# Kernel tuning notes

Measured on AMD Instinct MI355X. Metric: run time of the kernel, lower is better.

The kernel has to match this reference:

```python
import jax, jax.numpy as jnp
import numpy as np

B, N, C = 8, 89, 1024
H = C // 2  # adaptor hidden dim = channel_in // 2


def _mlp2(t, W1, b1, W2, b2):
    # MLP(channel_in, [channel_in, channel_out]): Linear -> ReLU -> Linear
    return jax.nn.relu(t @ W1 + b1) @ W2 + b2


def setup_inputs() -> dict:
    key = jax.random.key(0)
    ks = jax.random.split(key, 12)
    g = lambda k, shape, fan: jax.random.normal(k, shape, jnp.float32) * (fan ** -0.5)
    return {
        "x": jax.random.normal(ks[0], (B, N, C), jnp.float32),
        # two independently learned dense adjacencies (AddConv / ModulatorConv)
        "adj_add": jax.random.normal(ks[1], (N, N), jnp.float32),
        "adj_mod": jax.random.normal(ks[2], (N, N), jnp.float32),
        # Adaptor MLP: C -> C -> H -> 1
        "Wa1": g(ks[3], (C, C), C), "ba1": jnp.zeros((C,), jnp.float32),
        "Wa2": g(ks[4], (C, H), C), "ba2": jnp.zeros((H,), jnp.float32),
        "Wa3": g(ks[5], (H, 1), H), "ba3": jnp.zeros((1,), jnp.float32),
        # mlp_add: C -> C -> C
        "Wadd1": g(ks[6], (C, C), C), "badd1": jnp.zeros((C,), jnp.float32),
        "Wadd2": g(ks[7], (C, C), C), "badd2": jnp.zeros((C,), jnp.float32),
        # mlp_mod: C -> C -> C
        "Wmod1": g(ks[8], (C, C), C), "bmod1": jnp.zeros((C,), jnp.float32),
        "Wmod2": g(ks[9], (C, C), C), "bmod2": jnp.zeros((C,), jnp.float32),
    }


def reference(x, adj_add, adj_mod, Wa1, ba1, Wa2, ba2, Wa3, ba3,
              Wadd1, badd1, Wadd2, badd2, Wmod1, bmod1, Wmod2, bmod2):
    # dense_to_sparse on an all-nonzero learned randn adj => fully connected graph;
    # PyG convention: edge_index[0]=row=source j, edge_index[1]=col=target i,
    # so aggregation at node i sums over adj[j, i] * message(j -> i).

    # Adaptor: per-edge gate s_{b,j,i} = sigmoid(MLP(x_j * x_i))
    p = x[:, :, None, :] * x[:, None, :, :]              # [B, Nsrc, Ndst, C]
    h = jax.nn.relu(p @ Wa1 + ba1)                       # [B, N, N, C]
    h = jax.nn.relu(h @ Wa2 + ba2)                       # [B, N, N, H]
    s = jax.nn.sigmoid((h @ Wa3 + ba3)[..., 0])          # [B, Nsrc, Ndst]

    # AddConv: out[b,i,f] = sum_j s[b,j,i] * adj_add[j,i] * x[b,j,f]
    a_t = jnp.einsum('bji,ji,bjf->bif', s, adj_add, x)
    # ModulatorConv: out[b,i,f] = x[b,i,f] * sum_j adj_mod[j,i] * x[b,j,f]
    m_t = x * jnp.einsum('ji,bjf->bif', adj_mod, x)

    out_add = _mlp2(a_t, Wadd1, badd1, Wadd2, badd2)
    out_mod = _mlp2(m_t, Wmod1, bmod1, Wmod2, bmod2)
    return (x + out_add + out_mod) / 3.0
```

## Files before the change

### kernel.cpp

```cpp
#include <hip/hip_runtime.h>

typedef unsigned short u16;
typedef unsigned int   u32;
typedef __attribute__((ext_vector_type(8))) short bf16x8;
typedef __attribute__((ext_vector_type(4))) float f32x4;

#define DEVFN __device__ __forceinline__

DEVFN float b2f(u16 u){ u32 t=((u32)u)<<16; float f; __builtin_memcpy(&f,&t,4); return f; }
DEVFN u16 f2b(float f){ u32 t; __builtin_memcpy(&t,&f,4); t += 0x7fffu + ((t>>16)&1u); return (u16)(t>>16); }
DEVFN u32 pk2(float a, float b){ return (u32)f2b(a) | ((u32)f2b(b)<<16); }

DEVFN void row2ji(int row, int* jj, int* ii){
  int j = (int)((179.0f - sqrtf(179.0f*179.0f - 8.0f*(float)row)) * 0.5f);
  if(j < 0) j = 0; if(j > 88) j = 88;
  while(j < 88 && (j+1)*(179-(j+1))/2 <= row) j++;
  while(j > 0 && j*(179-j)/2 > row) j--;
  *jj = j;
  *ii = j + (row - j*(179-j)/2);
}

struct TrArgs { const float* src; u16* dst; int C; };
struct TrPack { TrArgs a[6]; };

__global__ __launch_bounds__(256) void prep_k(TrPack pk, float* __restrict__ logit,
                                              float* __restrict__ dout,
                                              const float* __restrict__ x,
                                              u16* __restrict__ pbuf, long pz){
  __shared__ u16 tile[32][33];
  int id = blockIdx.x, tid = threadIdx.x;
  if(id < 6144){
    TrArgs t = pk.a[id>>10];
    int q = id & 1023;
    int bx = (q&31)*32, by = (q>>5)*32;
    if(bx >= t.C) return;
    int tx = tid&31, ty = tid>>5;
    #pragma unroll
    for(int yy=ty; yy<32; yy+=8) tile[yy][tx] = f2b(t.src[(size_t)(by+yy)*t.C + bx+tx]);
    __syncthreads();
    #pragma unroll
    for(int yy=ty; yy<32; yy+=8) t.dst[(size_t)(bx+yy)*1024 + by+tx] = tile[tx][yy];
  } else if(id < 6176){
    int idx = (id-6144)*1024 + tid*4;
    *(float4*)(logit + idx) = (float4){0.f,0.f,0.f,0.f};
  } else if(id < 6888){
    int idx = (id-6176)*1024 + tid*4;
    *(float4*)(dout + idx) = (float4){0.f,0.f,0.f,0.f};
  } else {
    int pid = id - 6888;
    int z = pid >> 11, rp = pid & 2047;
    int half = tid >> 7, t7 = tid & 127;
    int row = rp*2 + half;
    int j, i; row2ji(row < 4005 ? row : 0, &j, &i);
    const float* xb = x + (size_t)z*91136;
    int c = t7*8;
    float4 a0 = *(const float4*)(xb + (size_t)j*1024 + c);
    float4 a1 = *(const float4*)(xb + (size_t)j*1024 + c + 4);
    float4 b0 = *(const float4*)(xb + (size_t)i*1024 + c);
    float4 b1 = *(const float4*)(xb + (size_t)i*1024 + c + 4);
    uint4 o;
    o.x = pk2(a0.x*b0.x, a0.y*b0.y);
    o.y = pk2(a0.z*b0.z, a0.w*b0.w);
    o.z = pk2(a1.x*b1.x, a1.y*b1.y);
    o.w = pk2(a1.z*b1.z, a1.w*b1.w);
    *(uint4*)(pbuf + (size_t)z*pz + (size_t)row*1024 + c) = o;
  }
}

__global__ __launch_bounds__(256) void pgen_k(const float* __restrict__ x,
                                              u16* __restrict__ p, long pz, int bbase){
  int z = blockIdx.y, b = bbase + z, row = blockIdx.x;
  int j, i; row2ji(row < 4005 ? row : 0, &j, &i);
  const float* xb = x + (size_t)b*91136;
  int c = threadIdx.x*4;
  float4 a  = *(const float4*)(xb + (size_t)j*1024 + c);
  float4 bb = *(const float4*)(xb + (size_t)i*1024 + c);
  ushort4 o;
  o.x = f2b(a.x*bb.x); o.y = f2b(a.y*bb.y);
  o.z = f2b(a.z*bb.z); o.w = f2b(a.w*bb.w);
  *(ushort4*)(p + (size_t)z*pz + (size_t)row*1024 + c) = o;
}

template<int ROWS>
DEVFN void stage_gl(const u16* __restrict__ g0, u16* lds0, int tid){
  constexpr int IT = ROWS/32;
  int w = tid>>6, lane = tid&63;
  #pragma unroll
  for(int i=0;i<IT;i++){
    int p  = (w*IT+i)*64 + lane;
    int r  = p>>3;
    int kb = (p&7) ^ (r&7);
    const u16* g = g0 + ((size_t)r<<10) + (kb<<3);
    u16* l = lds0 + (size_t)(w*IT+i)*512;
    __builtin_amdgcn_global_load_lds((const __attribute__((address_space(1))) u32*)g,
                                     (__attribute__((address_space(3))) u32*)l, 16, 0, 0);
  }
}

template<int AMODE, int EPI, int TM, int TN, int MINW>
__global__ __launch_bounds__(256,MINW) void gemm_k(
    const u16* __restrict__ A0, const u16* __restrict__ B0,
    const u16* __restrict__ A1, const u16* __restrict__ B1,
    const float* __restrict__ bias0, const float* __restrict__ bias1,
    const float* __restrict__ aux,
    void* __restrict__ out,
    long a0z, long oz, int ldo, int aux2, int kiters,
    int mmask, int mshift, int mlimit)
{
  constexpr int MB = TM/32, NB = TN/32;
  int by = blockIdx.y;
  int m0 = (by & mmask)*TM, n0 = (by >> mshift)*TN, z = blockIdx.z;
  if(m0 >= mlimit) return;

  __shared__ __align__(16) u16 smem[TM*64 + TN*64];
  u16* As = smem;
  u16* Bs = smem + TM*64;
  int tid = threadIdx.x;

  const u16* Abase0;
  const u16* Bbase0;
  if(AMODE==2){
    Abase0 = (z ? A1 : A0) + (size_t)m0*1024;
    Bbase0 = (z ? B1 : B0) + (size_t)n0*1024;
  } else {
    Abase0 = A0 + (size_t)z*a0z + (size_t)m0*1024;
    Bbase0 = B0 + (size_t)n0*1024;
  }

  f32x4 acc[MB][NB];
  #pragma unroll
  for(int a=0;a<MB;a++)
    #pragma unroll
    for(int b=0;b<NB;b++) acc[a][b] = (f32x4){0.f,0.f,0.f,0.f};

  int w = tid>>6, lane = tid&63, quad = lane>>4, l15 = lane&15;
  int wr = (w>>1)*(TM/2), wc = (w&1)*(TN/2);

  for(int kk=0; kk<kiters; kk++){
    int k0 = (kk & 15) << 6;
    const u16* Ab = Abase0 + k0;
    const u16* Bb = Bbase0 + k0;
    __syncthreads();
    stage_gl<TM>(Ab, As, tid);
    stage_gl<TN>(Bb, Bs, tid);
    __syncthreads();
    #pragma unroll
    for(int kq=0; kq<2; kq++){
      int kbl = kq*4 + quad;
      bf16x8 af[MB], bfv[NB];
      #pragma unroll
      for(int t=0;t<MB;t++){
        int rr = wr + t*16 + l15;
        af[t] = *(const bf16x8*)(As + rr*64 + ((kbl ^ (rr&7))<<3));
      }
      #pragma unroll
      for(int t=0;t<NB;t++){
        int cc = wc + t*16 + l15;
        bfv[t] = *(const bf16x8*)(Bs + cc*64 + ((kbl ^ (cc&7))<<3));
      }
      #pragma unroll
      for(int rt=0;rt<MB;rt++)
        #pragma unroll
        for(int ct=0;ct<NB;ct++)
          acc[rt][ct] = __builtin_amdgcn_mfma_f32_16x16x32_bf16(af[rt], bfv[ct], acc[rt][ct], 0,0,0);
    }
  }

  float bc[NB], w3[NB];
  #pragma unroll
  for(int ct=0;ct<NB;ct++){
    int colg = n0 + wc + ct*16 + l15;
    if(EPI==3){
      bc[ct] = (z==0) ? (bias0[colg] + bias1[colg]) : 0.f;
    } else {
      bc[ct] = (AMODE==2 && z) ? bias1[colg] : bias0[colg];
      if(EPI==2) w3[ct] = aux[colg];
    }
  }

  if(EPI==2){
    float part[MB][4];
    #pragma unroll
    for(int rt=0;rt<MB;rt++)
      #pragma unroll
      for(int r=0;r<4;r++) part[rt][r] = 0.f;
    #pragma unroll
    for(int rt=0;rt<MB;rt++)
      #pragma unroll
      for(int ct=0;ct<NB;ct++)
        #pragma unroll
        for(int r=0;r<4;r++)
          part[rt][r] += fmaxf(acc[rt][ct][r] + bc[ct], 0.f) * w3[ct];
    #pragma unroll
    for(int m=1;m<16;m<<=1)
      #pragma unroll
      for(int rt=0;rt<MB;rt++)
        #pragma unroll
        for(int r=0;r<4;r++)
          part[rt][r] += __shfl_xor(part[rt][r], m, 64);
    if(l15==0){
      float* lo = (float*)out + (size_t)(aux2 + z)*4096;
      #pragma unroll
      for(int rt=0;rt<MB;rt++)
        #pragma unroll
        for(int r=0;r<4;r++)
          atomicAdd(lo + (m0 + wr + rt*16 + quad*4 + r), part[rt][r]);
    }
    return;
  }

  if(EPI==3){
    const float third = 1.f/3.f;
    float* op = (float*)out;
    #pragma unroll
    for(int ct=0;ct<NB;ct++){
      int colg = n0 + wc + ct*16 + l15;
      #pragma unroll
      for(int rt=0;rt<MB;rt++){
        #pragma unroll
        for(int r=0;r<4;r++){
          int rowg = m0 + wr + rt*16 + quad*4 + r;
          if(rowg < aux2){
            float v = acc[rt][ct][r];
            if(z==0) v += aux[(size_t)rowg*1024 + colg] + bc[ct];
            atomicAdd(op + (size_t)rowg*ldo + colg, v*third);
          }
        }
      }
    }
    return;
  }

  __syncthreads();
  u16* Ct = smem;
  #pragma unroll
  for(int ct=0;ct<NB;ct++){
    int cl = wc + ct*16 + l15;
    #pragma unroll
    for(int rt=0;rt<MB;rt++){
      #pragma unroll
      for(int r=0;r<4;r++){
        int rl = wr + rt*16 + quad*4 + r;
        Ct[rl*TN + cl] = f2b(fmaxf(acc[rt][ct][r] + bc[ct], 0.f));
      }
    }
  }
  __syncthreads();
  u16* outp = (u16*)out + (size_t)z*oz;
  #pragma unroll
  for(int i=0;i<TM*TN/2048;i++){
    int q = i*256 + tid;
    int row = q/(TN/8), c16 = q%(TN/8);
    *(uint4*)(outp + (size_t)(m0+row)*ldo + n0 + c16*8) = *(const uint4*)(Ct + row*TN + c16*8);
  }
}

__global__ __launch_bounds__(256) void k4_k(const float* __restrict__ x,
    const float* __restrict__ adjA, const float* __restrict__ adjM,
    const float* __restrict__ logit, const float* __restrict__ ba3,
    u16* __restrict__ a_t, u16* __restrict__ m_t)
{
  int b = blockIdx.y, i = blockIdx.x, t = threadIdx.x;
  __shared__ float ca[89], cm[89];
  if(t < 89){
    int tri = (t<=i) ? t*(179-t)/2 + (i-t) : i*(179-i)/2 + (t-i);
    float lg = logit[(size_t)b*4096 + tri] + ba3[0];
    float sv = 1.f/(1.f + expf(-lg));
    ca[t] = sv * adjA[t*89 + i];
    cm[t] = adjM[t*89 + i];
  }
  __syncthreads();
  const float* xb = x + (size_t)b*91136;
  int c0 = t*4;
  float aa0=0,aa1=0,aa2=0,aa3=0, am0=0,am1=0,am2=0,am3=0;
  #pragma unroll 8
  for(int j=0;j<89;j++){
    float4 xv = *(const float4*)(xb + (size_t)j*1024 + c0);
    float fa=ca[j], fm=cm[j];
    aa0+=fa*xv.x; aa1+=fa*xv.y; aa2+=fa*xv.z; aa3+=fa*xv.w;
    am0+=fm*xv.x; am1+=fm*xv.y; am2+=fm*xv.z; am3+=fm*xv.w;
  }
  float4 xi = *(const float4*)(xb + (size_t)i*1024 + c0);
  size_t ro = ((size_t)(b*89 + i))*1024 + c0;
  ushort4 oa; oa.x=f2b(aa0); oa.y=f2b(aa1); oa.z=f2b(aa2); oa.w=f2b(aa3);
  ushort4 om;
  om.x=f2b(xi.x*am0); om.y=f2b(xi.y*am1);
  om.z=f2b(xi.z*am2); om.w=f2b(xi.w*am3);
  *(ushort4*)(a_t + ro) = oa;
  *(ushort4*)(m_t + ro) = om;
}

extern "C" void kernel_launch(void* const* d_in, const int* in_sizes, int n_in,
                              void* d_out, int out_size, void* d_ws, size_t ws_size,
                              hipStream_t stream)
{
  const float* X     = (const float*)d_in[0];
  const float* adjA  = (const float*)d_in[1];
  const float* adjM  = (const float*)d_in[2];
  const float* Wa1   = (const float*)d_in[3];
  const float* ba1   = (const float*)d_in[4];
  const float* Wa2   = (const float*)d_in[5];
  const float* ba2   = (const float*)d_in[6];
  const float* Wa3   = (const float*)d_in[7];
  const float* ba3   = (const float*)d_in[8];
  const float* Wadd1 = (const float*)d_in[9];
  const float* badd1 = (const float*)d_in[10];
  const float* Wadd2 = (const float*)d_in[11];
  const float* badd2 = (const float*)d_in[12];
  const float* Wmod1 = (const float*)d_in[13];
  const float* bmod1 = (const float*)d_in[14];
  const float* Wmod2 = (const float*)d_in[15];
  const float* bmod2 = (const float*)d_in[16];

  char* w = (char*)d_ws;
  u16* WaT1   = (u16*)w; w += (size_t)1024*1024*2;
  u16* WaT2   = (u16*)w; w += (size_t)512*1024*2;
  u16* WaddT1 = (u16*)w; w += (size_t)1024*1024*2;
  u16* WaddT2 = (u16*)w; w += (size_t)1024*1024*2;
  u16* WmodT1 = (u16*)w; w += (size_t)1024*1024*2;
  u16* WmodT2 = (u16*)w; w += (size_t)1024*1024*2;
  float* logit= (float*)w; w += (size_t)8*4096*4;
  u16* a_t    = (u16*)w; w += (size_t)768*1024*2;
  u16* m_t    = (u16*)w; w += (size_t)768*1024*2;
  u16* ha     = (u16*)w; w += (size_t)768*1024*2;
  u16* hm     = (u16*)w; w += (size_t)768*1024*2;
  size_t fixed = (size_t)(w - (char*)d_ws);
  size_t per_p = (size_t)4096*1024*2, per_h1 = (size_t)4096*1024*2;
  bool flat = ws_size >= fixed + 8*(per_p + per_h1);
  int nb = flat ? 8 : 1;
  u16* pbuf = (u16*)w; w += per_p  * nb;
  u16* h1   = (u16*)w;

  TrPack tp;
  tp.a[0].src = Wa1;   tp.a[0].dst = WaT1;   tp.a[0].C = 1024;
  tp.a[1].src = Wa2;   tp.a[1].dst = WaT2;   tp.a[1].C = 512;
  tp.a[2].src = Wadd1; tp.a[2].dst = WaddT1; tp.a[2].C = 1024;
  tp.a[3].src = Wadd2; tp.a[3].dst = WaddT2; tp.a[3].C = 1024;
  tp.a[4].src = Wmod1; tp.a[4].dst = WmodT1; tp.a[4].C = 1024;
  tp.a[5].src = Wmod2; tp.a[5].dst = WmodT2; tp.a[5].C = 1024;

  long pz = 4096*1024, h1z = 4096*1024;
  prep_k<<<dim3(6888 + 2048*nb), 256, 0, stream>>>(tp, logit, (float*)d_out, X, pbuf, pz);

  for(int bb=0; bb<8; bb+=nb){
    if(bb) pgen_k<<<dim3(4096,nb),256,0,stream>>>(X, pbuf, pz, bb);
    gemm_k<0,0,128,128,3><<<dim3(1,256,nb),256,0,stream>>>(pbuf, WaT1, nullptr,nullptr, ba1,nullptr, nullptr,
                                                           h1, pz, h1z, 1024, 4096, 16, 31, 5, 4096);
    gemm_k<0,2,128,256,2><<<dim3(1,64,nb),256,0,stream>>>(h1, WaT2, nullptr,nullptr, ba2,nullptr, Wa3,
                                                          logit, h1z, 0, 0, bb, 16, 31, 5, 4096);
  }
  k4_k<<<dim3(89,8),256,0,stream>>>(X, adjA, adjM, logit, ba3, a_t, m_t);
  gemm_k<2,0,64,64,4><<<dim3(1,256,2),256,0,stream>>>(a_t, WaddT1, m_t, WmodT1, badd1, bmod1, nullptr,
                                                      ha, 0, (long)768*1024, 1024, 768, 16, 15, 4, 768);
  gemm_k<2,3,64,64,4><<<dim3(1,256,2),256,0,stream>>>(ha, WaddT2, hm, WmodT2, badd2, bmod2, X,
                                                      d_out, 0, 0, 1024, 712, 16, 15, 4, 768);
}
```

Baseline: 270.3 us.

## Fuse all stages into one persistent kernel with atomic grid barriers

Replaces the sequence of separate kernel launches (prep, two adaptor GEMMs, k4 aggregation, two MLP GEMMs) with a single persistent kernel of 768 blocks that grid-strides over each stage's work and synchronises stages with a spin-wait atomic global barrier. The goal is to remove kernel launch gaps and tail effects between stages. The second adaptor GEMM also switches from 128x256 to 128x128 tiles so it shares the same LDS buffer. The cost is one occupancy/tile configuration for every stage, spin barriers whose cost grows with grid size, and a deadlock risk if the 768 blocks are not all co-resident at 3 blocks per CU.

```diff
diff --git a/kernel.cpp b/kernel.cpp
--- a/kernel.cpp
+++ b/kernel.cpp
@@ -6,6 +6,7 @@
 typedef __attribute__((ext_vector_type(4))) float f32x4;
 
 #define DEVFN __device__ __forceinline__
+#define GRID 768
 
 DEVFN float b2f(u16 u){ u32 t=((u32)u)<<16; float f; __builtin_memcpy(&f,&t,4); return f; }
 DEVFN u16 f2b(float f){ u32 t; __builtin_memcpy(&t,&f,4); t += 0x7fffu + ((t>>16)&1u); return (u16)(t>>16); }
@@ -23,23 +24,34 @@
 struct TrArgs { const float* src; u16* dst; int C; };
 struct TrPack { TrArgs a[6]; };
 
-__global__ __launch_bounds__(256) void prep_k(TrPack pk, float* __restrict__ logit,
-                                              float* __restrict__ dout,
-                                              const float* __restrict__ x,
-                                              u16* __restrict__ pbuf, long pz){
-  __shared__ u16 tile[32][33];
-  int id = blockIdx.x, tid = threadIdx.x;
+DEVFN void gbar(u32* cnt, u32 target){
+  __syncthreads();
+  if(threadIdx.x == 0){
+    __threadfence();
+    __hip_atomic_fetch_add(cnt, 1u, __ATOMIC_RELEASE, __HIP_MEMORY_SCOPE_AGENT);
+    while(__hip_atomic_load(cnt, __ATOMIC_ACQUIRE, __HIP_MEMORY_SCOPE_AGENT) < target)
+      __builtin_amdgcn_s_sleep(8);
+    __threadfence();
+  }
+  __syncthreads();
+}
+
+DEVFN void prep_body(const TrPack& pk, float* __restrict__ logit, float* __restrict__ dout,
+                     const float* __restrict__ x, u16* __restrict__ pbuf, long pz,
+                     int id, int tid, u16* tile ){
   if(id < 6144){
     TrArgs t = pk.a[id>>10];
     int q = id & 1023;
     int bx = (q&31)*32, by = (q>>5)*32;
-    if(bx >= t.C) return;
-    int tx = tid&31, ty = tid>>5;
-    #pragma unroll
-    for(int yy=ty; yy<32; yy+=8) tile[yy][tx] = f2b(t.src[(size_t)(by+yy)*t.C + bx+tx]);
-    __syncthreads();
-    #pragma unroll
-    for(int yy=ty; yy<32; yy+=8) t.dst[(size_t)(bx+yy)*1024 + by+tx] = tile[tx][yy];
+    if(bx < t.C){
+      int tx = tid&31, ty = tid>>5;
+      #pragma unroll
+      for(int yy=ty; yy<32; yy+=8) tile[yy*33+tx] = f2b(t.src[(size_t)(by+yy)*t.C + bx+tx]);
+      __syncthreads();
+      #pragma unroll
+      for(int yy=ty; yy<32; yy+=8) t.dst[(size_t)(bx+yy)*1024 + by+tx] = tile[tx*33+yy];
+      __syncthreads();
+    }
   } else if(id < 6176){
     int idx = (id-6144)*1024 + tid*4;
     *(float4*)(logit + idx) = (float4){0.f,0.f,0.f,0.f};
@@ -67,20 +79,6 @@
   }
 }
 
-__global__ __launch_bounds__(256) void pgen_k(const float* __restrict__ x,
-                                              u16* __restrict__ p, long pz, int bbase){
-  int z = blockIdx.y, b = bbase + z, row = blockIdx.x;
-  int j, i; row2ji(row < 4005 ? row : 0, &j, &i);
-  const float* xb = x + (size_t)b*91136;
-  int c = threadIdx.x*4;
-  float4 a  = *(const float4*)(xb + (size_t)j*1024 + c);
-  float4 bb = *(const float4*)(xb + (size_t)i*1024 + c);
-  ushort4 o;
-  o.x = f2b(a.x*bb.x); o.y = f2b(a.y*bb.y);
-  o.z = f2b(a.z*bb.z); o.w = f2b(a.w*bb.w);
-  *(ushort4*)(p + (size_t)z*pz + (size_t)row*1024 + c) = o;
-}
-
 template<int ROWS>
 DEVFN void stage_gl(const u16* __restrict__ g0, u16* lds0, int tid){
   constexpr int IT = ROWS/32;
@@ -97,25 +95,18 @@
   }
 }
 
-template<int AMODE, int EPI, int TM, int TN, int MINW>
-__global__ __launch_bounds__(256,MINW) void gemm_k(
+template<int AMODE, int EPI, int TM, int TN>
+DEVFN void gemm_tile(
     const u16* __restrict__ A0, const u16* __restrict__ B0,
     const u16* __restrict__ A1, const u16* __restrict__ B1,
     const float* __restrict__ bias0, const float* __restrict__ bias1,
-    const float* __restrict__ aux,
-    void* __restrict__ out,
-    long a0z, long oz, int ldo, int aux2, int kiters,
-    int mmask, int mshift, int mlimit)
+    const float* __restrict__ aux, void* __restrict__ out,
+    long a0z, long oz, int ldo, int aux2,
+    int m0, int n0, int z, u16* smem, int tid)
 {
   constexpr int MB = TM/32, NB = TN/32;
-  int by = blockIdx.y;
-  int m0 = (by & mmask)*TM, n0 = (by >> mshift)*TN, z = blockIdx.z;
-  if(m0 >= mlimit) return;
-
-  __shared__ __align__(16) u16 smem[TM*64 + TN*64];
   u16* As = smem;
   u16* Bs = smem + TM*64;
-  int tid = threadIdx.x;
 
   const u16* Abase0;
   const u16* Bbase0;
@@ -136,13 +127,11 @@
   int w = tid>>6, lane = tid&63, quad = lane>>4, l15 = lane&15;
   int wr = (w>>1)*(TM/2), wc = (w&1)*(TN/2);
 
-  for(int kk=0; kk<kiters; kk++){
-    int k0 = (kk & 15) << 6;
-    const u16* Ab = Abase0 + k0;
-    const u16* Bb = Bbase0 + k0;
+  for(int kk=0; kk<16; kk++){
+    int k0 = kk << 6;
     __syncthreads();
-    stage_gl<TM>(Ab, As, tid);
-    stage_gl<TN>(Bb, Bs, tid);
+    stage_gl<TM>(Abase0 + k0, As, tid);
+    stage_gl<TN>(Bbase0 + k0, Bs, tid);
     __syncthreads();
     #pragma unroll
     for(int kq=0; kq<2; kq++){
@@ -255,22 +244,21 @@
   }
 }
 
-__global__ __launch_bounds__(256) void k4_k(const float* __restrict__ x,
+DEVFN void k4_body(const float* __restrict__ x,
     const float* __restrict__ adjA, const float* __restrict__ adjM,
     const float* __restrict__ logit, const float* __restrict__ ba3,
-    u16* __restrict__ a_t, u16* __restrict__ m_t)
+    u16* __restrict__ a_t, u16* __restrict__ m_t,
+    int bz, int i, int t, float* ca, float* cm)
 {
-  int b = blockIdx.y, i = blockIdx.x, t = threadIdx.x;
-  __shared__ float ca[89], cm[89];
   if(t < 89){
     int tri = (t<=i) ? t*(179-t)/2 + (i-t) : i*(179-i)/2 + (t-i);
-    float lg = logit[(size_t)b*4096 + tri] + ba3[0];
+    float lg = logit[(size_t)bz*4096 + tri] + ba3[0];
     float sv = 1.f/(1.f + expf(-lg));
     ca[t] = sv * adjA[t*89 + i];
     cm[t] = adjM[t*89 + i];
   }
   __syncthreads();
-  const float* xb = x + (size_t)b*91136;
+  const float* xb = x + (size_t)bz*91136;
   int c0 = t*4;
   float aa0=0,aa1=0,aa2=0,aa3=0, am0=0,am1=0,am2=0,am3=0;
   #pragma unroll 8
@@ -281,13 +269,114 @@
     am0+=fm*xv.x; am1+=fm*xv.y; am2+=fm*xv.z; am3+=fm*xv.w;
   }
   float4 xi = *(const float4*)(xb + (size_t)i*1024 + c0);
-  size_t ro = ((size_t)(b*89 + i))*1024 + c0;
+  size_t ro = ((size_t)(bz*89 + i))*1024 + c0;
   ushort4 oa; oa.x=f2b(aa0); oa.y=f2b(aa1); oa.z=f2b(aa2); oa.w=f2b(aa3);
   ushort4 om;
   om.x=f2b(xi.x*am0); om.y=f2b(xi.y*am1);
   om.z=f2b(xi.z*am2); om.w=f2b(xi.w*am3);
   *(ushort4*)(a_t + ro) = oa;
   *(ushort4*)(m_t + ro) = om;
+  __syncthreads();
+}
+
+struct MegaArgs {
+  TrPack tp;
+  float* logit; float* dout;
+  const float* X; const float* adjA; const float* adjM;
+  const float *ba1,*ba2,*Wa3,*ba3,*badd1,*bmod1,*badd2,*bmod2;
+  u16 *WaT1,*WaT2,*WaddT1,*WaddT2,*WmodT1,*WmodT2;
+  u16 *a_t,*m_t,*ha,*hm,*pbuf,*h1;
+  u32* cnt;
+};
+
+__global__ __launch_bounds__(256,3) void mega_k(MegaArgs a){
+  __shared__ __align__(16) u16 smem[(128+128)*64];
+  int b = blockIdx.x, tid = threadIdx.x;
+  const long pz = (long)4096*1024, h1z = (long)4096*1024;
+
+  for(int id=b; id<23272; id+=GRID)
+    prep_body(a.tp, a.logit, a.dout, a.X, a.pbuf, pz, id, tid, smem);
+  gbar(a.cnt, 1*GRID);
+
+  for(int v=b; v<2048; v+=GRID){
+    int n = v>>8, p = v&255, z = p>>5, m = p&31;
+    gemm_tile<0,0,128,128>(a.pbuf, a.WaT1, nullptr,nullptr, a.ba1,nullptr, nullptr,
+                           a.h1, pz, h1z, 1024, 0, m*128, n*128, z, smem, tid);
+  }
+  gbar(a.cnt, 2*GRID);
+
+  for(int v=b; v<1024; v+=GRID){
+    int n = v>>8, p = v&255, z = p>>5, m = p&31;
+    gemm_tile<0,2,128,128>(a.h1, a.WaT2, nullptr,nullptr, a.ba2,nullptr, a.Wa3,
+                           a.logit, h1z, 0, 0, 0, m*128, n*128, z, smem, tid);
+  }
+  gbar(a.cnt, 3*GRID);
+
+  for(int id=b; id<712; id+=GRID)
+    k4_body(a.X, a.adjA, a.adjM, a.logit, a.ba3, a.a_t, a.m_t,
+            id/89, id%89, tid, (float*)smem, (float*)smem + 96);
+  gbar(a.cnt, 4*GRID);
+
+  if(b < 384){
+    int z = b/192, rem = b%192, m = rem%12, n = rem/12;
+    gemm_tile<2,0,64,64>(a.a_t, a.WaddT1, a.m_t, a.WmodT1, a.badd1, a.bmod1, nullptr,
+                         a.ha, 0, (long)768*1024, 1024, 0, m*64, n*64, z, smem, tid);
+  }
+  gbar(a.cnt, 5*GRID);
+
+  if(b < 384){
+    int z = b/192, rem = b%192, m = rem%12, n = rem/12;
+    gemm_tile<2,3,64,64>(a.ha, a.WaddT2, a.hm, a.WmodT2, a.badd2, a.bmod2, a.X,
+                         a.dout, 0, 0, 1024, 712, m*64, n*64, z, smem, tid);
+  }
+}
+
+__global__ __launch_bounds__(256) void prep_k(TrPack pk, float* __restrict__ logit,
+                                              float* __restrict__ dout,
+                                              const float* __restrict__ x,
+                                              u16* __restrict__ pbuf, long pz){
+  __shared__ u16 tile[32*33];
+  prep_body(pk, logit, dout, x, pbuf, pz, blockIdx.x, threadIdx.x, tile);
+}
+
+__global__ __launch_bounds__(256) void pgen_k(const float* __restrict__ x,
+                                              u16* __restrict__ p, long pz, int bbase){
+  int z = blockIdx.y, b = bbase + z, row = blockIdx.x;
+  int j, i; row2ji(row < 4005 ? row : 0, &j, &i);
+  const float* xb = x + (size_t)b*91136;
+  int c = threadIdx.x*4;
+  float4 a  = *(const float4*)(xb + (size_t)j*1024 + c);
+  float4 bb = *(const float4*)(xb + (size_t)i*1024 + c);
+  ushort4 o;
+  o.x = f2b(a.x*bb.x); o.y = f2b(a.y*bb.y);
+  o.z = f2b(a.z*bb.z); o.w = f2b(a.w*bb.w);
+  *(ushort4*)(p + (size_t)z*pz + (size_t)row*1024 + c) = o;
+}
+
+template<int AMODE, int EPI, int TM, int TN, int MINW>
+__global__ __launch_bounds__(256,MINW) void gemm_k(
+    const u16* __restrict__ A0, const u16* __restrict__ B0,
+    const u16* __restrict__ A1, const u16* __restrict__ B1,
+    const float* __restrict__ bias0, const float* __restrict__ bias1,
+    const float* __restrict__ aux, void* __restrict__ out,
+    long a0z, long oz, int ldo, int aux2,
+    int mmask, int mshift, int mlimit)
+{
+  int by = blockIdx.y;
+  int m0 = (by & mmask)*TM, n0 = (by >> mshift)*TN, z = blockIdx.z;
+  if(m0 >= mlimit) return;
+  __shared__ __align__(16) u16 smem[(TM+TN)*64];
+  gemm_tile<AMODE,EPI,TM,TN>(A0,B0,A1,B1,bias0,bias1,aux,out,a0z,oz,ldo,aux2,
+                             m0,n0,z,smem,threadIdx.x);
+}
+
+__global__ __launch_bounds__(256) void k4_k(const float* __restrict__ x,
+    const float* __restrict__ adjA, const float* __restrict__ adjM,
+    const float* __restrict__ logit, const float* __restrict__ ba3,
+    u16* __restrict__ a_t, u16* __restrict__ m_t)
+{
+  __shared__ float ca[96], cm[96];
+  k4_body(x, adjA, adjM, logit, ba3, a_t, m_t, blockIdx.y, blockIdx.x, threadIdx.x, ca, cm);
 }
 
 extern "C" void kernel_launch(void* const* d_in, const int* in_sizes, int n_in,
@@ -324,6 +413,7 @@
   u16* m_t    = (u16*)w; w += (size_t)768*1024*2;
   u16* ha     = (u16*)w; w += (size_t)768*1024*2;
   u16* hm     = (u16*)w; w += (size_t)768*1024*2;
+  u32* cnt    = (u32*)w; w += 64;
   size_t fixed = (size_t)(w - (char*)d_ws);
   size_t per_p = (size_t)4096*1024*2, per_h1 = (size_t)4096*1024*2;
   bool flat = ws_size >= fixed + 8*(per_p + per_h1);
@@ -339,19 +429,34 @@
   tp.a[4].src = Wmod1; tp.a[4].dst = WmodT1; tp.a[4].C = 1024;
   tp.a[5].src = Wmod2; tp.a[5].dst = WmodT2; tp.a[5].C = 1024;
 
-  long pz = 4096*1024, h1z = 4096*1024;
+  long pz = (long)4096*1024, h1z = (long)4096*1024;
+
+  if(flat){
+    MegaArgs ma;
+    ma.tp = tp; ma.logit = logit; ma.dout = (float*)d_out;
+    ma.X = X; ma.adjA = adjA; ma.adjM = adjM;
+    ma.ba1 = ba1; ma.ba2 = ba2; ma.Wa3 = Wa3; ma.ba3 = ba3;
+    ma.badd1 = badd1; ma.bmod1 = bmod1; ma.badd2 = badd2; ma.bmod2 = bmod2;
+    ma.WaT1 = WaT1; ma.WaT2 = WaT2; ma.WaddT1 = WaddT1; ma.WaddT2 = WaddT2;
+    ma.WmodT1 = WmodT1; ma.WmodT2 = WmodT2;
+    ma.a_t = a_t; ma.m_t = m_t; ma.ha = ha; ma.hm = hm; ma.pbuf = pbuf; ma.h1 = h1;
+    ma.cnt = cnt;
+    hipMemsetAsync(cnt, 0, 64, stream);
+    mega_k<<<dim3(GRID), dim3(256), 0, stream>>>(ma);
+    return;
+  }
+
   prep_k<<<dim3(6888 + 2048*nb), 256, 0, stream>>>(tp, logit, (float*)d_out, X, pbuf, pz);
-
   for(int bb=0; bb<8; bb+=nb){
     if(bb) pgen_k<<<dim3(4096,nb),256,0,stream>>>(X, pbuf, pz, bb);
     gemm_k<0,0,128,128,3><<<dim3(1,256,nb),256,0,stream>>>(pbuf, WaT1, nullptr,nullptr, ba1,nullptr, nullptr,
-                                                           h1, pz, h1z, 1024, 4096, 16, 31, 5, 4096);
+                                                           h1, pz, h1z, 1024, 0, 31, 5, 4096);
     gemm_k<0,2,128,256,2><<<dim3(1,64,nb),256,0,stream>>>(h1, WaT2, nullptr,nullptr, ba2,nullptr, Wa3,
-                                                          logit, h1z, 0, 0, bb, 16, 31, 5, 4096);
+                                                          logit, h1z, 0, 0, bb, 31, 5, 4096);
   }
   k4_k<<<dim3(89,8),256,0,stream>>>(X, adjA, adjM, logit, ba3, a_t, m_t);
   gemm_k<2,0,64,64,4><<<dim3(1,256,2),256,0,stream>>>(a_t, WaddT1, m_t, WmodT1, badd1, bmod1, nullptr,
-                                                      ha, 0, (long)768*1024, 1024, 768, 16, 15, 4, 768);
+                                                      ha, 0, (long)768*1024, 1024, 0, 15, 4, 768);
   gemm_k<2,3,64,64,4><<<dim3(1,256,2),256,0,stream>>>(ha, WaddT2, hm, WmodT2, badd2, bmod2, X,
-                                                      d_out, 0, 0, 1024, 712, 16, 15, 4, 768);
-}
+                                                      d_out, 0, 0, 1024, 712, 15, 4, 768);
+}
```

Measured after the change: 1.052 ms. 289% more time.
